# Kernel optimization log

Measured on AMD Instinct MI355X. Metric: run time of the kernel, lower is better.

Reference implementation:

```python
import jax, jax.numpy as jnp
import numpy as np

B, T, C, P = 512, 365, 10, 64  # batch, num_steps, input_dim, num_prototypes


def setup_inputs() -> dict:
    key = jax.random.key(0)
    k1, k2, k3, k4 = jax.random.split(key, 4)
    input_seq = jax.random.normal(k1, (B, T, C), dtype=jnp.float32)
    # binary observation mask (some dates missing)
    mask = (jax.random.uniform(k2, (B, T)) > 0.1).astype(jnp.float32)
    label = jax.random.randint(k3, (B,), 0, P)
    prototypes = jax.random.normal(k4, (P, T, C), dtype=jnp.float32)
    return {"input_seq": input_seq, "mask": mask, "label": label,
            "prototypes": prototypes}


def reference(input_seq, mask, label, prototypes):
    # distances[b,p] = sum_{t,c} mask[b,t] * (x[b,t,c] - proto[p,t,c])^2
    # expanded so we never materialize the [B,P,T,C] broadcast:
    #   = sum mask*x^2  - 2*sum mask*x*p + sum mask*p^2
    x2 = jnp.einsum('btc,btc,bt->b', input_seq, input_seq, mask)          # [B]
    xp = jnp.einsum('btc,bt,ptc->bp', input_seq, mask, prototypes)        # [B,P]
    p2 = jnp.einsum('bt,ptc,ptc->bp', mask, prototypes, prototypes)       # [B,P]
    distances = x2[:, None] - 2.0 * xp + p2                               # [B,P]
    indices = jnp.argmin(distances, axis=1)                               # [B]
    # gather selected prototype per sample (trans/offset inactive -> shared protos)
    output_seq = prototypes[indices]                                      # [B,T,C]
    return (output_seq, input_seq, distances, indices, label, mask)
```

## Files before the change

kernel.cpp:

```cpp
#include <hip/hip_runtime.h>

#define B_  512
#define T_  365
#define C_  10
#define P_  64
#define K_  3650
#define K2_ 1825
#define KP_ 3712

#define OFF_OUT0 0u
#define OFF_IN   1868800u
#define OFF_DIST 3737600u
#define OFF_IDX  3770368u
#define OFF_LAB  3770880u
#define OFF_MASK 3771392u

__global__ __launch_bounds__(1024) void dist_kernel(
    const float* __restrict__ x, const float* __restrict__ mask,
    const int* __restrict__ label, const float* __restrict__ protos,
    float* __restrict__ out)
{
    __shared__ float xm[2][KP_];
    __shared__ float mexp[2][KP_];
    __shared__ float mrow[2][368];
    __shared__ float dist[2][64];
    __shared__ int   sel[2];

    const int tid  = threadIdx.x;
    const int lane = tid & 63;
    const int wv   = tid >> 6;
    const int b0   = blockIdx.x * 2;

    if (tid < T_) {
        float m = mask[(size_t)b0 * T_ + tid];
        mrow[0][tid] = m;
        out[OFF_MASK + (size_t)b0 * T_ + tid] = m;
    }
    {
        int t2 = tid - 512;
        if (t2 >= 0 && t2 < T_) {
            float m = mask[(size_t)(b0 + 1) * T_ + t2];
            mrow[1][t2] = m;
            out[OFF_MASK + (size_t)(b0 + 1) * T_ + t2] = m;
        }
    }
    __syncthreads();

    for (int i = tid; i < KP_; i += 1024) {
#pragma unroll
        for (int bb = 0; bb < 2; ++bb) {
            float m = 0.f, v = 0.f;
            if (i < K_) {
                float xv = x[(size_t)(b0 + bb) * K_ + i];
                out[OFF_IN + (size_t)(b0 + bb) * K_ + i] = xv;
                m = mrow[bb][i / C_];
                v = xv * m;
            }
            xm[bb][i]   = v;
            mexp[bb][i] = m;
        }
    }
    __syncthreads();

    const int p0 = wv * 4;
    const float2* pr[4];
#pragma unroll
    for (int q = 0; q < 4; ++q)
        pr[q] = (const float2*)(protos + (size_t)(p0 + q) * K_);
    const float2* xr0 = (const float2*)&xm[0][0];
    const float2* xr1 = (const float2*)&xm[1][0];
    const float2* mr0 = (const float2*)&mexp[0][0];
    const float2* mr1 = (const float2*)&mexp[1][0];

    float acc0[4] = {0.f, 0.f, 0.f, 0.f};
    float acc1[4] = {0.f, 0.f, 0.f, 0.f};

#pragma unroll 4
    for (int it = 0; it < 29; ++it) {
        const int i2  = it * 64 + lane;
        const int i2c = i2 < K2_ ? i2 : (K2_ - 1);
        float2 pv[4];
#pragma unroll
        for (int q = 0; q < 4; ++q) pv[q] = pr[q][i2c];
        const float2 u0 = xr0[i2], m0 = mr0[i2];
        const float2 u1 = xr1[i2], m1 = mr1[i2];
#pragma unroll
        for (int q = 0; q < 4; ++q) {
            float tx, ty;
            tx = fmaf(-pv[q].x, m0.x, u0.x); acc0[q] = fmaf(tx, tx, acc0[q]);
            ty = fmaf(-pv[q].y, m0.y, u0.y); acc0[q] = fmaf(ty, ty, acc0[q]);
            tx = fmaf(-pv[q].x, m1.x, u1.x); acc1[q] = fmaf(tx, tx, acc1[q]);
            ty = fmaf(-pv[q].y, m1.y, u1.y); acc1[q] = fmaf(ty, ty, acc1[q]);
        }
    }

#pragma unroll
    for (int q = 0; q < 4; ++q) {
        float v0 = acc0[q], v1 = acc1[q];
        for (int off = 32; off; off >>= 1) {
            v0 += __shfl_down(v0, off);
            v1 += __shfl_down(v1, off);
        }
        if (lane == 0) {
            dist[0][p0 + q] = v0;
            dist[1][p0 + q] = v1;
        }
    }
    __syncthreads();

    if (tid < 128) {
        int bb = tid >> 6;
        out[OFF_DIST + (size_t)(b0 + bb) * P_ + lane] = dist[bb][lane];
    }
    if (wv < 2) {
        const int bb = wv;
        float v = dist[bb][lane];
        int idx = lane;
        for (int off = 32; off; off >>= 1) {
            float ov = __shfl_down(v, off);
            int   oi = __shfl_down(idx, off);
            if (ov < v || (ov == v && oi < idx)) { v = ov; idx = oi; }
        }
        if (lane == 0) {
            sel[bb] = idx;
            const int b = b0 + bb;
            out[OFF_IDX + b] = (float)idx;
            out[OFF_LAB + b] = (float)label[b];
        }
    }
    __syncthreads();

#pragma unroll
    for (int bb = 0; bb < 2; ++bb) {
        const float2* src = (const float2*)(protos + (size_t)sel[bb] * K_);
        float2* dst = (float2*)(out + OFF_OUT0 + (size_t)(b0 + bb) * K_);
        for (int i2 = tid; i2 < K2_; i2 += 1024) dst[i2] = src[i2];
    }
}

extern "C" void kernel_launch(void* const* d_in, const int* in_sizes, int n_in,
                              void* d_out, int out_size, void* d_ws, size_t ws_size,
                              hipStream_t stream) {
    const float* x      = (const float*)d_in[0];
    const float* mask   = (const float*)d_in[1];
    const int*   label  = (const int*)d_in[2];
    const float* protos = (const float*)d_in[3];
    float* out = (float*)d_out;

    dist_kernel<<<B_ / 2, 1024, 0, stream>>>(x, mask, label, protos, out);
}
```

Baseline: 88.53 us.

## Expand squared distance into dot product plus precomputed prototype norms

The per-element masked squared-difference loop is replaced by the expanded form x2 - 2*x·p + sum(mask*||p_t||^2). A new prep kernel pads prototypes to a float4-aligned layout in workspace and precomputes the per-timestep prototype squared norms. The inner loop becomes a pure float4 dot product with half the FMAs per element and no mask-expansion shared array. The cost is an extra kernel launch each call and a small risk of numerical differences that could flip argmin ties.

```diff
diff --git a/kernel.cpp b/kernel.cpp
--- a/kernel.cpp
+++ b/kernel.cpp
@@ -1,12 +1,14 @@
 #include <hip/hip_runtime.h>
 
-#define B_  512
-#define T_  365
-#define C_  10
-#define P_  64
-#define K_  3650
-#define K2_ 1825
-#define KP_ 3712
+#define B_   512
+#define T_   365
+#define C_   10
+#define P_   64
+#define K_   3650
+#define K2_  1825
+#define KP_  3712
+#define KP2_ 1856
+#define KP4_ 928
 
 #define OFF_OUT0 0u
 #define OFF_IN   1868800u
@@ -15,15 +17,39 @@
 #define OFF_LAB  3770880u
 #define OFF_MASK 3771392u
 
+#define WS_SP_OFF (P_ * KP_)
+
+__global__ __launch_bounds__(256) void prep_kernel(
+    const float* __restrict__ protos, float* __restrict__ ws)
+{
+    const int bid = blockIdx.x;
+    if (bid < 928) {
+        int j = bid * 256 + threadIdx.x;
+        int p = j / KP_;
+        int r = j - p * KP_;
+        ws[j] = (r < K_) ? protos[(size_t)p * K_ + r] : 0.f;
+    } else {
+        int i = (bid - 928) * 256 + threadIdx.x;
+        if (i < P_ * T_) {
+            const float* pp = protos + (size_t)i * C_;
+            float s = 0.f;
+#pragma unroll
+            for (int c = 0; c < C_; ++c) s = fmaf(pp[c], pp[c], s);
+            ws[WS_SP_OFF + i] = s;
+        }
+    }
+}
+
 __global__ __launch_bounds__(1024) void dist_kernel(
     const float* __restrict__ x, const float* __restrict__ mask,
     const int* __restrict__ label, const float* __restrict__ protos,
-    float* __restrict__ out)
+    const float* __restrict__ ws, float* __restrict__ out)
 {
     __shared__ float xm[2][KP_];
-    __shared__ float mexp[2][KP_];
     __shared__ float mrow[2][368];
     __shared__ float dist[2][64];
+    __shared__ float wsum[16][2];
+    __shared__ float x2s[2];
     __shared__ int   sel[2];
 
     const int tid  = threadIdx.x;
@@ -46,64 +72,92 @@
     }
     __syncthreads();
 
-    for (int i = tid; i < KP_; i += 1024) {
-#pragma unroll
-        for (int bb = 0; bb < 2; ++bb) {
-            float m = 0.f, v = 0.f;
-            if (i < K_) {
-                float xv = x[(size_t)(b0 + bb) * K_ + i];
-                out[OFF_IN + (size_t)(b0 + bb) * K_ + i] = xv;
-                m = mrow[bb][i / C_];
-                v = xv * m;
+    float s2[2] = {0.f, 0.f};
+#pragma unroll
+    for (int bb = 0; bb < 2; ++bb) {
+        const float2* xr = (const float2*)(x + (size_t)(b0 + bb) * K_);
+        float2*       er = (float2*)(out + OFF_IN + (size_t)(b0 + bb) * K_);
+        float2*       sm = (float2*)&xm[bb][0];
+        for (int i2 = tid; i2 < KP2_; i2 += 1024) {
+            float2 v = {0.f, 0.f};
+            if (i2 < K2_) {
+                v = xr[i2];
+                er[i2] = v;
+                int e = i2 * 2;
+                v.x *= mrow[bb][e / C_];
+                v.y *= mrow[bb][(e + 1) / C_];
             }
-            xm[bb][i]   = v;
-            mexp[bb][i] = m;
-        }
+            sm[i2] = v;
+            s2[bb] = fmaf(v.x, v.x, fmaf(v.y, v.y, s2[bb]));
+        }
+    }
+#pragma unroll
+    for (int bb = 0; bb < 2; ++bb) {
+        float v = s2[bb];
+        for (int off = 32; off; off >>= 1) v += __shfl_down(v, off);
+        if (lane == 0) wsum[wv][bb] = v;
+    }
+    __syncthreads();
+    if (tid < 2) {
+        float s = 0.f;
+#pragma unroll
+        for (int w = 0; w < 16; ++w) s += wsum[w][tid];
+        x2s[tid] = s;
     }
     __syncthreads();
 
     const int p0 = wv * 4;
-    const float2* pr[4];
-#pragma unroll
-    for (int q = 0; q < 4; ++q)
-        pr[q] = (const float2*)(protos + (size_t)(p0 + q) * K_);
-    const float2* xr0 = (const float2*)&xm[0][0];
-    const float2* xr1 = (const float2*)&xm[1][0];
-    const float2* mr0 = (const float2*)&mexp[0][0];
-    const float2* mr1 = (const float2*)&mexp[1][0];
+    const float4* pw  = (const float4*)ws;
+    const float4* xr0 = (const float4*)&xm[0][0];
+    const float4* xr1 = (const float4*)&xm[1][0];
 
     float acc0[4] = {0.f, 0.f, 0.f, 0.f};
     float acc1[4] = {0.f, 0.f, 0.f, 0.f};
 
-#pragma unroll 4
-    for (int it = 0; it < 29; ++it) {
-        const int i2  = it * 64 + lane;
-        const int i2c = i2 < K2_ ? i2 : (K2_ - 1);
-        float2 pv[4];
-#pragma unroll
-        for (int q = 0; q < 4; ++q) pv[q] = pr[q][i2c];
-        const float2 u0 = xr0[i2], m0 = mr0[i2];
-        const float2 u1 = xr1[i2], m1 = mr1[i2];
+#pragma unroll 5
+    for (int it = 0; it < 15; ++it) {
+        const int i4  = it * 64 + lane;
+        const bool ok = (i4 < KP4_);
+        const int i4c = ok ? i4 : 0;
+        float4 pv[4];
+#pragma unroll
+        for (int q = 0; q < 4; ++q)
+            pv[q] = pw[(size_t)(p0 + q) * KP4_ + i4c];
+        float4 u0 = xr0[i4c];
+        float4 u1 = xr1[i4c];
+        if (!ok) { u0.x=u0.y=u0.z=u0.w=0.f; u1.x=u1.y=u1.z=u1.w=0.f; }
 #pragma unroll
         for (int q = 0; q < 4; ++q) {
-            float tx, ty;
-            tx = fmaf(-pv[q].x, m0.x, u0.x); acc0[q] = fmaf(tx, tx, acc0[q]);
-            ty = fmaf(-pv[q].y, m0.y, u0.y); acc0[q] = fmaf(ty, ty, acc0[q]);
-            tx = fmaf(-pv[q].x, m1.x, u1.x); acc1[q] = fmaf(tx, tx, acc1[q]);
-            ty = fmaf(-pv[q].y, m1.y, u1.y); acc1[q] = fmaf(ty, ty, acc1[q]);
-        }
-    }
-
+            acc0[q] = fmaf(u0.x, pv[q].x, acc0[q]);
+            acc0[q] = fmaf(u0.y, pv[q].y, acc0[q]);
+            acc0[q] = fmaf(u0.z, pv[q].z, acc0[q]);
+            acc0[q] = fmaf(u0.w, pv[q].w, acc0[q]);
+            acc1[q] = fmaf(u1.x, pv[q].x, acc1[q]);
+            acc1[q] = fmaf(u1.y, pv[q].y, acc1[q]);
+            acc1[q] = fmaf(u1.z, pv[q].z, acc1[q]);
+            acc1[q] = fmaf(u1.w, pv[q].w, acc1[q]);
+        }
+    }
+
+    const float* sp = ws + WS_SP_OFF;
 #pragma unroll
     for (int q = 0; q < 4; ++q) {
-        float v0 = acc0[q], v1 = acc1[q];
+        const float* spq = sp + (size_t)(p0 + q) * T_;
+        float c0 = 0.f, c1 = 0.f;
+        for (int t = lane; t < T_; t += 64) {
+            float s = spq[t];
+            c0 = fmaf(s, mrow[0][t], c0);
+            c1 = fmaf(s, mrow[1][t], c1);
+        }
+        float v0 = fmaf(-2.f, acc0[q], c0);
+        float v1 = fmaf(-2.f, acc1[q], c1);
         for (int off = 32; off; off >>= 1) {
             v0 += __shfl_down(v0, off);
             v1 += __shfl_down(v1, off);
         }
         if (lane == 0) {
-            dist[0][p0 + q] = v0;
-            dist[1][p0 + q] = v1;
+            dist[0][p0 + q] = x2s[0] + v0;
+            dist[1][p0 + q] = x2s[1] + v1;
         }
     }
     __syncthreads();
@@ -146,6 +200,8 @@
     const int*   label  = (const int*)d_in[2];
     const float* protos = (const float*)d_in[3];
     float* out = (float*)d_out;
-
-    dist_kernel<<<B_ / 2, 1024, 0, stream>>>(x, mask, label, protos, out);
+    float* ws  = (float*)d_ws;
+
+    prep_kernel<<<1020, 256, 0, stream>>>(protos, ws);
+    dist_kernel<<<B_ / 2, 1024, 0, stream>>>(x, mask, label, protos, ws, out);
 }
```

Result: slower. 100.2 us (+13.2%).
